# Kernel optimization log

Measured on AMD Instinct MI355X. Metric: run time of the kernel, lower is better.

## Reference

```python
import jax, jax.numpy as jnp
import numpy as np
from jax import lax

KX = jnp.array([[-1., 0., 1.], [-2., 0., 2.], [-1., 0., 1.]], dtype=jnp.float32)
KY = jnp.array([[1., 2., 1.], [0., 0., 0.], [-1., -2., -1.]], dtype=jnp.float32)


def _dwconv3(x, k):
    # x: [B,C,H,W]; k: [3,3]; depthwise 3x3 cross-correlation, padding=1 (matches torch F.conv2d)
    C = x.shape[1]
    kern = jnp.broadcast_to(k.astype(x.dtype)[None, None], (C, 1, 3, 3))
    return lax.conv_general_dilated(
        x, kern, window_strides=(1, 1), padding='SAME',
        dimension_numbers=('NCHW', 'OIHW', 'NCHW'), feature_group_count=C)


def _sobel(x):
    # |sobel_x| + |sobel_y|, shape [B,C,H,W] (the original adds a size-1 K dim, squeezed/kept trivially)
    return jnp.abs(_dwconv3(x, KX)) + jnp.abs(_dwconv3(x, KY))


def setup_inputs() -> dict:
    key = jax.random.key(0)
    ks = jax.random.split(key, 4)
    shape = (16, 1, 768, 768)
    return {
        'image_vis': jax.random.uniform(ks[0], shape, dtype=jnp.float32),
        'image_ir': jax.random.uniform(ks[1], shape, dtype=jnp.float32),
        'image_X': jax.random.uniform(ks[2], shape, dtype=jnp.float32),
        'image_Y': jax.random.uniform(ks[3], shape, dtype=jnp.float32),
    }


def reference(image_vis, image_ir, image_X, image_Y):
    # loss_in = mean(sobel(Y)^2) / mean(sobel(X)^2)
    x_size = jnp.mean(jnp.square(_sobel(image_X)))
    y_size = jnp.mean(jnp.square(_sobel(image_Y)))
    loss_in = y_size / x_size

    y_grad = _sobel(image_vis)
    ir_grad = _sobel(image_ir)          # broadcast replaces .expand
    gen_grad = _sobel(image_X)
    joint = jnp.maximum(y_grad, ir_grad)
    loss_grad = jnp.mean(jnp.abs(gen_grad - joint))  # F.l1_loss
    return (loss_in, loss_grad)
```

## Files before the change

### kernel.cpp

```cpp
#include <hip/hip_runtime.h>
#include <math.h>

#define IMG_H 768
#define IMG_W 768
#define BATCH 16
#define TPB 256
#define XSPAN 256
#define NBX (IMG_W / XSPAN)
#define NBY (IMG_H / 4)
#define NBLOCKS (NBX * NBY * BATCH)
#define NPIX ((size_t)BATCH * IMG_H * IMG_W)

__global__ __launch_bounds__(TPB) void sobel_loss_main(
    const float* __restrict__ vis, const float* __restrict__ ir,
    const float* __restrict__ X, const float* __restrict__ Y,
    float* __restrict__ part)
{
    __shared__ float red[3][4];

    const int tid  = threadIdx.x;
    const int lane = tid & 63;
    const int wv   = tid >> 6;
    const int x0   = blockIdx.x * XSPAN + lane * 4;
    const int y    = blockIdx.y * 4 + wv;
    const size_t base = (size_t)blockIdx.z * (IMG_H * IMG_W);
    const int bid = (blockIdx.z * NBY + blockIdx.y) * NBX + blockIdx.x;

    const float* img[4] = { vis + base, ir + base, X + base, Y + base };

    const bool e0  = (lane == 0)  && (x0 > 0);
    const bool e63 = (lane == 63) && (x0 + 4 < IMG_W);
    const int  eoff = e0 ? -1 : 4;

    float4 m[4][3];
    float  ev[4][3];
    #pragma unroll
    for (int im = 0; im < 4; ++im) {
        #pragma unroll
        for (int dy = 0; dy < 3; ++dy) {
            int row = y + dy - 1;
            int rc  = row < 0 ? 0 : (row > IMG_H - 1 ? IMG_H - 1 : row);
            m[im][dy] = *(const float4*)(img[im] + rc * IMG_W + x0);
        }
    }
    #pragma unroll
    for (int im = 0; im < 4; ++im) {
        #pragma unroll
        for (int dy = 0; dy < 3; ++dy) {
            int row = y + dy - 1;
            int rc  = row < 0 ? 0 : (row > IMG_H - 1 ? IMG_H - 1 : row);
            float e = 0.f;
            if (e0 | e63) e = (img[im] + rc * IMG_W + x0)[eoff];
            ev[im][dy] = e;
        }
    }
    __builtin_amdgcn_sched_barrier(0);

    float g[4][4];
    #pragma unroll
    for (int im = 0; im < 4; ++im) {
        float r[3][6];
        #pragma unroll
        for (int dy = 0; dy < 3; ++dy) {
            float msk;
            if (dy == 1) msk = 1.f;
            else {
                int row = y + dy - 1;
                msk = (row >= 0 && row < IMG_H) ? 1.f : 0.f;
            }
            float4 mm = m[im][dy];
            float  e  = ev[im][dy];
            float left  = __shfl_up(mm.w, 1);
            float right = __shfl_down(mm.x, 1);
            if (lane == 0)  left  = e;
            if (lane == 63) right = e;
            r[dy][0] = left  * msk;
            r[dy][1] = mm.x * msk;
            r[dy][2] = mm.y * msk;
            r[dy][3] = mm.z * msk;
            r[dy][4] = mm.w * msk;
            r[dy][5] = right * msk;
        }
        #pragma unroll
        for (int jj = 0; jj < 4; ++jj) {
            float gx = (r[0][jj + 2] - r[0][jj]) + 2.f * (r[1][jj + 2] - r[1][jj]) + (r[2][jj + 2] - r[2][jj]);
            float gy = (r[0][jj] - r[2][jj]) + 2.f * (r[0][jj + 1] - r[2][jj + 1]) + (r[0][jj + 2] - r[2][jj + 2]);
            g[im][jj] = fabsf(gx) + fabsf(gy);
        }
    }

    float sX2 = 0.f, sY2 = 0.f, sL1 = 0.f;
    #pragma unroll
    for (int jj = 0; jj < 4; ++jj) {
        float jnt = fmaxf(g[0][jj], g[1][jj]);
        float gX = g[2][jj], gY = g[3][jj];
        sX2 += gX * gX;
        sY2 += gY * gY;
        sL1 += fabsf(gX - jnt);
    }

    #pragma unroll
    for (int off = 32; off > 0; off >>= 1) {
        sX2 += __shfl_down(sX2, off);
        sY2 += __shfl_down(sY2, off);
        sL1 += __shfl_down(sL1, off);
    }
    if (lane == 0) { red[0][wv] = sX2; red[1][wv] = sY2; red[2][wv] = sL1; }
    __syncthreads();
    if (tid == 0) {
        part[0 * NBLOCKS + bid] = red[0][0] + red[0][1] + red[0][2] + red[0][3];
        part[1 * NBLOCKS + bid] = red[1][0] + red[1][1] + red[1][2] + red[1][3];
        part[2 * NBLOCKS + bid] = red[2][0] + red[2][1] + red[2][2] + red[2][3];
    }
}

__global__ __launch_bounds__(1024) void reduce_finalize(
    const float* __restrict__ part, float* __restrict__ out)
{
    __shared__ float red[3][16];
    const int tid = threadIdx.x;

    float a = 0.f, b = 0.f, c = 0.f;
    for (int i = tid; i < NBLOCKS; i += 1024) {
        a += part[0 * NBLOCKS + i];
        b += part[1 * NBLOCKS + i];
        c += part[2 * NBLOCKS + i];
    }
    #pragma unroll
    for (int off = 32; off > 0; off >>= 1) {
        a += __shfl_down(a, off);
        b += __shfl_down(b, off);
        c += __shfl_down(c, off);
    }
    const int wave = tid >> 6;
    const int lane = tid & 63;
    if (lane == 0) { red[0][wave] = a; red[1][wave] = b; red[2][wave] = c; }
    __syncthreads();
    if (tid == 0) {
        float sa = 0.f, sb = 0.f, sc = 0.f;
        #pragma unroll
        for (int w = 0; w < 16; ++w) { sa += red[0][w]; sb += red[1][w]; sc += red[2][w]; }
        out[0] = sb / sa;
        out[1] = sc * (1.f / (float)NPIX);
    }
}

extern "C" void kernel_launch(void* const* d_in, const int* in_sizes, int n_in,
                              void* d_out, int out_size, void* d_ws, size_t ws_size,
                              hipStream_t stream) {
    const float* vis = (const float*)d_in[0];
    const float* ir  = (const float*)d_in[1];
    const float* X   = (const float*)d_in[2];
    const float* Y   = (const float*)d_in[3];
    float* out = (float*)d_out;
    float* part = (float*)d_ws;

    dim3 grid(NBX, NBY, BATCH);
    sobel_loss_main<<<grid, TPB, 0, stream>>>(vis, ir, X, Y, part);
    reduce_finalize<<<1, 1024, 0, stream>>>(part, out);
}
```

Measured before the change: 47.15 us.

## Stage full-width row strips in LDS via direct global-to-LDS loads

Each block now covers a full-width strip of 4 rows for one batch image. It loads 6 halo rows for all four images straight into LDS with global_load_lds, one wave per image, and each thread then computes 12 horizontal pixels from LDS. This is meant to cut the 3x redundant row reads from global memory and the per-lane edge loads of the earlier scheme. In exchange it uses about 72KB of LDS per block, which limits occupancy to roughly one or two blocks per CU, and it adds a block barrier before compute, reducing load/compute overlap.

```diff
diff --git a/kernel.cpp b/kernel.cpp
--- a/kernel.cpp
+++ b/kernel.cpp
@@ -4,99 +4,121 @@
 #define IMG_H 768
 #define IMG_W 768
 #define BATCH 16
+#define TH 4
 #define TPB 256
-#define XSPAN 256
-#define NBX (IMG_W / XSPAN)
-#define NBY (IMG_H / 4)
-#define NBLOCKS (NBX * NBY * BATCH)
+#define NSTRIPS (IMG_H / TH)
+#define NBLOCKS (NSTRIPS * BATCH)
 #define NPIX ((size_t)BATCH * IMG_H * IMG_W)
+
+typedef const __attribute__((address_space(1))) float* gp1_t;
+typedef __attribute__((address_space(3))) float* lp3_t;
 
 __global__ __launch_bounds__(TPB) void sobel_loss_main(
     const float* __restrict__ vis, const float* __restrict__ ir,
     const float* __restrict__ X, const float* __restrict__ Y,
     float* __restrict__ part)
 {
+    __shared__ __align__(16) float lds[4][TH + 2][IMG_W];
     __shared__ float red[3][4];
 
     const int tid  = threadIdx.x;
     const int lane = tid & 63;
     const int wv   = tid >> 6;
-    const int x0   = blockIdx.x * XSPAN + lane * 4;
-    const int y    = blockIdx.y * 4 + wv;
-    const size_t base = (size_t)blockIdx.z * (IMG_H * IMG_W);
-    const int bid = (blockIdx.z * NBY + blockIdx.y) * NBX + blockIdx.x;
+    const int y0   = blockIdx.x * TH;
+    const size_t base = (size_t)blockIdx.y * (IMG_H * IMG_W);
+    const int bid = blockIdx.y * NSTRIPS + blockIdx.x;
 
     const float* img[4] = { vis + base, ir + base, X + base, Y + base };
 
-    const bool e0  = (lane == 0)  && (x0 > 0);
-    const bool e63 = (lane == 63) && (x0 + 4 < IMG_W);
-    const int  eoff = e0 ? -1 : 4;
+    {
+        const float* ip = img[wv];
+        #pragma unroll
+        for (int i = 0; i < 3 * (TH + 2); ++i) {
+            const int row = i / 3, seg = i % 3;
+            int gr = y0 - 1 + row;
+            int rc = gr < 0 ? 0 : (gr > IMG_H - 1 ? IMG_H - 1 : gr);
+            const float* src = ip + (size_t)rc * IMG_W + seg * 256 + lane * 4;
+            __builtin_amdgcn_global_load_lds((gp1_t)src, (lp3_t)&lds[wv][row][seg * 256], 16, 0, 0);
+        }
+    }
+    __syncthreads();
 
-    float4 m[4][3];
-    float  ev[4][3];
+    if (y0 == 0) {
+        for (int i = tid; i < IMG_W; i += TPB) {
+            lds[0][0][i] = 0.f; lds[1][0][i] = 0.f; lds[2][0][i] = 0.f; lds[3][0][i] = 0.f;
+        }
+        __syncthreads();
+    } else if (y0 + TH == IMG_H) {
+        for (int i = tid; i < IMG_W; i += TPB) {
+            lds[0][TH + 1][i] = 0.f; lds[1][TH + 1][i] = 0.f; lds[2][TH + 1][i] = 0.f; lds[3][TH + 1][i] = 0.f;
+        }
+        __syncthreads();
+    }
+
+    const int r0 = wv, r1 = wv + 1, r2 = wv + 2;
+    const int xb = lane * 12;
+
+    float jnt[12];
+    float sX2 = 0.f, sY2 = 0.f, sL1 = 0.f;
+
     #pragma unroll
     for (int im = 0; im < 4; ++im) {
+        float4 t0 = *(const float4*)&lds[im][r0][xb];
+        float4 t1 = *(const float4*)&lds[im][r0][xb + 4];
+        float4 t2 = *(const float4*)&lds[im][r0][xb + 8];
+        float4 m0 = *(const float4*)&lds[im][r1][xb];
+        float4 m1 = *(const float4*)&lds[im][r1][xb + 4];
+        float4 m2 = *(const float4*)&lds[im][r1][xb + 8];
+        float4 b0 = *(const float4*)&lds[im][r2][xb];
+        float4 b1 = *(const float4*)&lds[im][r2][xb + 4];
+        float4 b2 = *(const float4*)&lds[im][r2][xb + 8];
+
+        float T[14], M[14], B[14];
+        T[1] = t0.x; T[2] = t0.y; T[3] = t0.z; T[4] = t0.w;
+        T[5] = t1.x; T[6] = t1.y; T[7] = t1.z; T[8] = t1.w;
+        T[9] = t2.x; T[10] = t2.y; T[11] = t2.z; T[12] = t2.w;
+        M[1] = m0.x; M[2] = m0.y; M[3] = m0.z; M[4] = m0.w;
+        M[5] = m1.x; M[6] = m1.y; M[7] = m1.z; M[8] = m1.w;
+        M[9] = m2.x; M[10] = m2.y; M[11] = m2.z; M[12] = m2.w;
+        B[1] = b0.x; B[2] = b0.y; B[3] = b0.z; B[4] = b0.w;
+        B[5] = b1.x; B[6] = b1.y; B[7] = b1.z; B[8] = b1.w;
+        B[9] = b2.x; B[10] = b2.y; B[11] = b2.z; B[12] = b2.w;
+
+        float tl = __shfl_up(t2.w, 1),  tr = __shfl_down(t0.x, 1);
+        float ml = __shfl_up(m2.w, 1),  mr = __shfl_down(m0.x, 1);
+        float bl = __shfl_up(b2.w, 1),  br = __shfl_down(b0.x, 1);
+        T[0] = (lane == 0) ? 0.f : tl;  T[13] = (lane == 63) ? 0.f : tr;
+        M[0] = (lane == 0) ? 0.f : ml;  M[13] = (lane == 63) ? 0.f : mr;
+        B[0] = (lane == 0) ? 0.f : bl;  B[13] = (lane == 63) ? 0.f : br;
+
+        float s[14], d[14];
         #pragma unroll
-        for (int dy = 0; dy < 3; ++dy) {
-            int row = y + dy - 1;
-            int rc  = row < 0 ? 0 : (row > IMG_H - 1 ? IMG_H - 1 : row);
-            m[im][dy] = *(const float4*)(img[im] + rc * IMG_W + x0);
+        for (int j = 0; j < 14; ++j) { s[j] = T[j] + B[j]; d[j] = T[j] - B[j]; }
+
+        float g[12];
+        #pragma unroll
+        for (int j = 0; j < 12; ++j) {
+            float gx = (s[j + 2] - s[j]) + 2.f * (M[j + 2] - M[j]);
+            float gy = d[j] + 2.f * d[j + 1] + d[j + 2];
+            g[j] = fabsf(gx) + fabsf(gy);
         }
-    }
-    #pragma unroll
-    for (int im = 0; im < 4; ++im) {
-        #pragma unroll
-        for (int dy = 0; dy < 3; ++dy) {
-            int row = y + dy - 1;
-            int rc  = row < 0 ? 0 : (row > IMG_H - 1 ? IMG_H - 1 : row);
-            float e = 0.f;
-            if (e0 | e63) e = (img[im] + rc * IMG_W + x0)[eoff];
-            ev[im][dy] = e;
+
+        if (im == 0) {
+            #pragma unroll
+            for (int j = 0; j < 12; ++j) jnt[j] = g[j];
+        } else if (im == 1) {
+            #pragma unroll
+            for (int j = 0; j < 12; ++j) jnt[j] = fmaxf(jnt[j], g[j]);
+        } else if (im == 2) {
+            #pragma unroll
+            for (int j = 0; j < 12; ++j) {
+                sX2 += g[j] * g[j];
+                sL1 += fabsf(g[j] - jnt[j]);
+            }
+        } else {
+            #pragma unroll
+            for (int j = 0; j < 12; ++j) sY2 += g[j] * g[j];
         }
-    }
-    __builtin_amdgcn_sched_barrier(0);
-
-    float g[4][4];
-    #pragma unroll
-    for (int im = 0; im < 4; ++im) {
-        float r[3][6];
-        #pragma unroll
-        for (int dy = 0; dy < 3; ++dy) {
-            float msk;
-            if (dy == 1) msk = 1.f;
-            else {
-                int row = y + dy - 1;
-                msk = (row >= 0 && row < IMG_H) ? 1.f : 0.f;
-            }
-            float4 mm = m[im][dy];
-            float  e  = ev[im][dy];
-            float left  = __shfl_up(mm.w, 1);
-            float right = __shfl_down(mm.x, 1);
-            if (lane == 0)  left  = e;
-            if (lane == 63) right = e;
-            r[dy][0] = left  * msk;
-            r[dy][1] = mm.x * msk;
-            r[dy][2] = mm.y * msk;
-            r[dy][3] = mm.z * msk;
-            r[dy][4] = mm.w * msk;
-            r[dy][5] = right * msk;
-        }
-        #pragma unroll
-        for (int jj = 0; jj < 4; ++jj) {
-            float gx = (r[0][jj + 2] - r[0][jj]) + 2.f * (r[1][jj + 2] - r[1][jj]) + (r[2][jj + 2] - r[2][jj]);
-            float gy = (r[0][jj] - r[2][jj]) + 2.f * (r[0][jj + 1] - r[2][jj + 1]) + (r[0][jj + 2] - r[2][jj + 2]);
-            g[im][jj] = fabsf(gx) + fabsf(gy);
-        }
-    }
-
-    float sX2 = 0.f, sY2 = 0.f, sL1 = 0.f;
-    #pragma unroll
-    for (int jj = 0; jj < 4; ++jj) {
-        float jnt = fmaxf(g[0][jj], g[1][jj]);
-        float gX = g[2][jj], gY = g[3][jj];
-        sX2 += gX * gX;
-        sY2 += gY * gY;
-        sL1 += fabsf(gX - jnt);
     }
 
     #pragma unroll
@@ -155,7 +177,7 @@
     float* out = (float*)d_out;
     float* part = (float*)d_ws;
 
-    dim3 grid(NBX, NBY, BATCH);
+    dim3 grid(NSTRIPS, BATCH);
     sobel_loss_main<<<grid, TPB, 0, stream>>>(vis, ir, X, Y, part);
     reduce_finalize<<<1, 1024, 0, stream>>>(part, out);
 }
```

Result: faster. 41.48 us (-12.0%).
